# Kernel tuning notes

Hardware: AMD Instinct MI355X
Metric: run time of the kernel (lower is better)

Reference implementation:

```python
import jax, jax.numpy as jnp
import numpy as np

N = 50000      # n_nodes
E = 800000     # n_edges (before self-loops)
IN = 256       # in_channels
MID = 512      # mid_channel
MID2 = MID // 2
OUT = 64       # out_channels


def setup_inputs() -> dict:
    key = jax.random.key(0)
    ks = jax.random.split(key, 16)
    def w(k, shape):
        fan_in = shape[0]
        return jax.random.normal(k, shape, jnp.float32) * (1.0 / np.sqrt(fan_in))
    return {
        "node_feature": jax.random.normal(ks[0], (N, IN), jnp.float32),
        "edge_index": jax.random.randint(ks[1], (2, E), 0, N, jnp.int32),
        # GCNConv weights (PyG convention: x @ W, bias added after aggregation)
        "Wg1": w(ks[2], (IN, MID)),   "bg1": jnp.zeros((MID,), jnp.float32),
        "Wg2": w(ks[3], (MID, MID2)), "bg2": jnp.zeros((MID2,), jnp.float32),
        "Wg3": w(ks[4], (MID2, OUT)), "bg3": jnp.zeros((OUT,), jnp.float32),
        # parallel Linear layers
        "Wl1": w(ks[5], (IN, MID)),   "bl1": jnp.zeros((MID,), jnp.float32),
        "Wl2": w(ks[6], (MID, MID2)), "bl2": jnp.zeros((MID2,), jnp.float32),
        "Wl3": w(ks[7], (MID2, OUT)), "bl3": jnp.zeros((OUT,), jnp.float32),
    }


def reference(node_feature, edge_index, Wg1, bg1, Wg2, bg2, Wg3, bg3,
              Wl1, bl1, Wl2, bl2, Wl3, bl3):
    n = node_feature.shape[0]
    # list_add_self_loops: append (i, i) for every node
    loops = jnp.arange(n, dtype=edge_index.dtype)
    src = jnp.concatenate([edge_index[0], loops])
    dst = jnp.concatenate([edge_index[1], loops])
    # symmetric GCN normalization: deg computed on graph with self-loops
    deg = jax.ops.segment_sum(jnp.ones_like(dst, jnp.float32), dst, num_segments=n)
    dis = jax.lax.rsqrt(jnp.maximum(deg, 1.0))  # deg >= 1 thanks to self-loops
    norm = dis[src] * dis[dst]                  # [E'] edge coefficients

    def gcn_conv(x, W, b):
        h = x @ W                                            # [N, F_out]
        msgs = h[src] * norm[:, None]                        # gather + scale
        return jax.ops.segment_sum(msgs, dst, num_segments=n) + b  # scatter-add

    h1 = jax.nn.elu(gcn_conv(node_feature, Wg1, bg1)) + node_feature @ Wl1 + bl1
    h2 = jax.nn.elu(gcn_conv(h1, Wg2, bg2)) + h1 @ Wl2 + bl2
    out = gcn_conv(h2, Wg3, bg3) + h2 @ Wl3 + bl3
    return out
```

## Files before the change

kernel.cpp:

```cpp
#include <hip/hip_runtime.h>
#include <hip/hip_bf16.h>
#include <math.h>

#define IN_CH  256
#define MID    512
#define MID2   256
#define OUT_CH 64

typedef __attribute__((ext_vector_type(8))) short s16x8;
typedef __attribute__((ext_vector_type(4))) float f32x4;


__global__ __launch_bounds__(256) void deg_kernel(const int* __restrict__ dst,
                                                  int* __restrict__ cnt, int E) {
  int stride = gridDim.x * blockDim.x;
  for (int e = blockIdx.x * blockDim.x + threadIdx.x; e < E; e += stride)
    atomicAdd(&cnt[dst[e]], 1);
}

__global__ __launch_bounds__(1024) void scan_dis_kernel(const int* __restrict__ cnt,
                                                        int* __restrict__ rowstart,
                                                        float* __restrict__ dis, int N) {
  __shared__ int part[1024];
  int t = threadIdx.x;
  int chunk = (N + 1023) >> 10;
  int lo = t * chunk;
  int hi = lo + chunk; if (hi > N) hi = N; if (lo > N) lo = N;
  int s = 0;
  for (int i = lo; i < hi; ++i) s += cnt[i] + 1;
  part[t] = s;
  __syncthreads();
  for (int off = 1; off < 1024; off <<= 1) {
    int v = (t >= off) ? part[t - off] : 0;
    __syncthreads();
    part[t] += v;
    __syncthreads();
  }
  int base = part[t] - s;
  for (int i = lo; i < hi; ++i) {
    int d = cnt[i] + 1;
    rowstart[i] = base;
    dis[i] = rsqrtf((float)d);
    base += d;
  }
  if (t == 1023) rowstart[N] = part[1023];
}

__global__ __launch_bounds__(256) void fill_adj_kernel(const int* __restrict__ src,
                                                       const int* __restrict__ dst,
                                                       const int* __restrict__ rowstart,
                                                       int* __restrict__ cnt2,
                                                       int* __restrict__ adj,
                                                       int E, int N) {
  int total = E + N;
  int stride = gridDim.x * blockDim.x;
  for (int e = blockIdx.x * blockDim.x + threadIdx.x; e < total; e += stride) {
    int s, d;
    if (e < E) { s = src[e]; d = dst[e]; }
    else       { s = d = e - E; }
    int pos = rowstart[d] + atomicAdd(&cnt2[d], 1);
    adj[pos] = s;
  }
}


__device__ inline unsigned bf16_rne(float v) {
  unsigned u = __float_as_uint(v);
  return (u + 0x7FFFu + ((u >> 16) & 1u)) >> 16;
}

__global__ __launch_bounds__(256) void wsplit_cat(const float* __restrict__ W,
                                                  short* __restrict__ Th,
                                                  short* __restrict__ Tl,
                                                  int K, int F, int noff) {
  int idx = blockIdx.x * 256 + threadIdx.x;
  if (idx >= K * F) return;
  int k = idx / F, n = idx - k * F;
  float v = W[idx];
  unsigned h = bf16_rne(v);
  float hf = __uint_as_float(h << 16);
  unsigned l = bf16_rne(v - hf);
  Th[(size_t)(noff + n) * K + k] = (short)h;
  Tl[(size_t)(noff + n) * K + k] = (short)l;
}


template<bool OUT2_BF16>
__global__ __launch_bounds__(256, 2)
void gemm_dual(const float* __restrict__ A, const short* __restrict__ Bth,
               const short* __restrict__ Btl, const float* __restrict__ bias1,
               float* __restrict__ C1, void* __restrict__ C2,
               int Nrows, int K, int F1) {
  __shared__ short lds[4 * 128 * 64];
  short* Ah = lds;
  short* Al = lds + 8192;
  short* Bh = lds + 16384;
  short* Bl = lds + 24576;

  const int tid  = threadIdx.x;
  const int lane = tid & 63;
  const int wid  = tid >> 6;
  const int wr = wid >> 1, wc = wid & 1;
  const int row0 = blockIdx.x * 128;
  const int col0 = blockIdx.y * 128;

  f32x4 acc[4][4] = {};

  const int sr    = tid >> 1;
  const int shalf = (tid & 1) << 5;
  int arow = row0 + sr; if (arow > Nrows - 1) arow = Nrows - 1;
  const float* Abase  = A   + (size_t)arow * K + shalf;
  const short* Bhbase = Bth + (size_t)(col0 + sr) * K + shalf;
  const short* Blbase = Btl + (size_t)(col0 + sr) * K + shalf;
  int wslot[4];
  #pragma unroll
  for (int i = 0; i < 4; ++i)
    wslot[i] = sr * 64 + ((((shalf >> 3) + i) ^ (sr & 7)) << 3);

  for (int k0 = 0; k0 < K; k0 += 64) {
    float4 av[8];
    const float* ap = Abase + k0;
    #pragma unroll
    for (int i = 0; i < 8; ++i) av[i] = *(const float4*)(ap + i * 4);
    s16x8 rbh[4], rbl[4];
    const short* bp = Bhbase + k0;
    const short* bq = Blbase + k0;
    #pragma unroll
    for (int i = 0; i < 4; ++i) rbh[i] = *(const s16x8*)(bp + i * 8);
    #pragma unroll
    for (int i = 0; i < 4; ++i) rbl[i] = *(const s16x8*)(bq + i * 8);

    __syncthreads();

    #pragma unroll
    for (int i = 0; i < 4; ++i) {
      s16x8 hi, lo;
      #pragma unroll
      for (int j = 0; j < 2; ++j) {
        float4 v = av[i * 2 + j];
        float vv[4] = {v.x, v.y, v.z, v.w};
        #pragma unroll
        for (int m = 0; m < 4; ++m) {
          unsigned h = bf16_rne(vv[m]);
          float hf = __uint_as_float(h << 16);
          unsigned l = bf16_rne(vv[m] - hf);
          hi[j * 4 + m] = (short)h;
          lo[j * 4 + m] = (short)l;
        }
      }
      *(s16x8*)(Ah + wslot[i]) = hi;
      *(s16x8*)(Al + wslot[i]) = lo;
    }
    #pragma unroll
    for (int i = 0; i < 4; ++i) {
      *(s16x8*)(Bh + wslot[i]) = rbh[i];
      *(s16x8*)(Bl + wslot[i]) = rbl[i];
    }
    __syncthreads();

    #pragma unroll
    for (int ks = 0; ks < 2; ++ks) {
      const int sw = ((((ks << 2) + (lane >> 4)) ^ (lane & 7)) << 3);
      s16x8 fah[4], fal[4], fbh[4], fbl[4];
      #pragma unroll
      for (int mi = 0; mi < 4; ++mi) {
        int base = (wr * 64 + mi * 16 + (lane & 15)) * 64 + sw;
        fah[mi] = *(const s16x8*)(Ah + base);
        fal[mi] = *(const s16x8*)(Al + base);
      }
      #pragma unroll
      for (int ni = 0; ni < 4; ++ni) {
        int base = (wc * 64 + ni * 16 + (lane & 15)) * 64 + sw;
        fbh[ni] = *(const s16x8*)(Bh + base);
        fbl[ni] = *(const s16x8*)(Bl + base);
      }
      #pragma unroll
      for (int mi = 0; mi < 4; ++mi)
        #pragma unroll
        for (int ni = 0; ni < 4; ++ni) {
          acc[mi][ni] = __builtin_amdgcn_mfma_f32_16x16x32_bf16(fah[mi], fbh[ni], acc[mi][ni], 0, 0, 0);
          acc[mi][ni] = __builtin_amdgcn_mfma_f32_16x16x32_bf16(fah[mi], fbl[ni], acc[mi][ni], 0, 0, 0);
          acc[mi][ni] = __builtin_amdgcn_mfma_f32_16x16x32_bf16(fal[mi], fbh[ni], acc[mi][ni], 0, 0, 0);
        }
    }
  }

  #pragma unroll
  for (int mi = 0; mi < 4; ++mi) {
    #pragma unroll
    for (int r = 0; r < 4; ++r) {
      int rr = row0 + wr * 64 + mi * 16 + (lane >> 4) * 4 + r;
      if (rr >= Nrows) continue;
      #pragma unroll
      for (int ni = 0; ni < 4; ++ni) {
        int cc = col0 + wc * 64 + ni * 16 + (lane & 15);
        float v = acc[mi][ni][r];
        if (cc < F1) {
          C1[(size_t)rr * F1 + cc] = v + bias1[cc];
        } else {
          int c2 = cc - F1;
          if (OUT2_BF16)
            ((unsigned short*)C2)[(size_t)rr * F1 + c2] = (unsigned short)bf16_rne(v);
          else
            ((float*)C2)[(size_t)rr * F1 + c2] = v;
        }
      }
    }
  }
}


template<int F, bool DO_ELU>
__global__ __launch_bounds__(256) void agg_bf16(const unsigned short* __restrict__ H,
                                                const int* __restrict__ adj,
                                                const int* __restrict__ rowstart,
                                                const float* __restrict__ dis,
                                                const float* __restrict__ bias,
                                                float* __restrict__ out, int N) {
  constexpr int VF = F / 64;
  typedef __attribute__((ext_vector_type(VF))) unsigned short uvec;
  int node = (int)((blockIdx.x * blockDim.x + threadIdx.x) >> 6);
  int lane = threadIdx.x & 63;
  if (node >= N) return;
  int e = rowstart[node];
  const int end = rowstart[node + 1];

  float acc[VF] = {};
  const unsigned short* base = H + (size_t)lane * VF;
  for (; e + 4 <= end; e += 4) {
    int s0 = adj[e], s1 = adj[e + 1], s2 = adj[e + 2], s3 = adj[e + 3];
    float w0 = dis[s0], w1 = dis[s1], w2 = dis[s2], w3 = dis[s3];
    uvec v0 = *(const uvec*)(base + (size_t)s0 * F);
    uvec v1 = *(const uvec*)(base + (size_t)s1 * F);
    uvec v2 = *(const uvec*)(base + (size_t)s2 * F);
    uvec v3 = *(const uvec*)(base + (size_t)s3 * F);
    #pragma unroll
    for (int j = 0; j < VF; ++j) {
      acc[j] = fmaf(__uint_as_float((unsigned)v0[j] << 16), w0, acc[j]);
      acc[j] = fmaf(__uint_as_float((unsigned)v1[j] << 16), w1, acc[j]);
      acc[j] = fmaf(__uint_as_float((unsigned)v2[j] << 16), w2, acc[j]);
      acc[j] = fmaf(__uint_as_float((unsigned)v3[j] << 16), w3, acc[j]);
    }
  }
  for (; e < end; ++e) {
    int s = adj[e]; float w = dis[s];
    uvec v = *(const uvec*)(base + (size_t)s * F);
    #pragma unroll
    for (int j = 0; j < VF; ++j)
      acc[j] = fmaf(__uint_as_float((unsigned)v[j] << 16), w, acc[j]);
  }

  float di = dis[node];
  float* op = out + (size_t)node * F + lane * VF;
  const float* bp = bias + lane * VF;
  #pragma unroll
  for (int j = 0; j < VF; ++j) {
    float val = fmaf(acc[j], di, bp[j]);
    if (DO_ELU) val = (val > 0.f) ? val : expm1f(val);
    op[j] += val;
  }
}


template<int F, bool DO_ELU>
__global__ __launch_bounds__(256) void agg_f32(const float* __restrict__ H,
                                               const int* __restrict__ adj,
                                               const int* __restrict__ rowstart,
                                               const float* __restrict__ dis,
                                               const float* __restrict__ bias,
                                               float* __restrict__ out, int N) {
  int node = (int)((blockIdx.x * blockDim.x + threadIdx.x) >> 6);
  int lane = threadIdx.x & 63;
  if (node >= N) return;
  int e = rowstart[node];
  const int end = rowstart[node + 1];
  float acc = 0.f;
  for (; e + 4 <= end; e += 4) {
    int s0 = adj[e], s1 = adj[e + 1], s2 = adj[e + 2], s3 = adj[e + 3];
    float w0 = dis[s0], w1 = dis[s1], w2 = dis[s2], w3 = dis[s3];
    float q0 = H[(size_t)s0 * F + lane], q1 = H[(size_t)s1 * F + lane];
    float q2 = H[(size_t)s2 * F + lane], q3 = H[(size_t)s3 * F + lane];
    acc = fmaf(q0, w0, acc); acc = fmaf(q1, w1, acc);
    acc = fmaf(q2, w2, acc); acc = fmaf(q3, w3, acc);
  }
  for (; e < end; ++e) {
    int s = adj[e];
    acc = fmaf(H[(size_t)s * F + lane], dis[s], acc);
  }
  float val = fmaf(acc, dis[node], bias[lane]);
  if (DO_ELU) val = (val > 0.f) ? val : expm1f(val);
  out[(size_t)node * F + lane] += val;
}


static inline char* ws_align(char*& ws, size_t bytes) {
  ws = (char*)(((uintptr_t)ws + 63) & ~(uintptr_t)63);
  char* p = ws;
  ws += bytes;
  return p;
}

extern "C" void kernel_launch(void* const* d_in, const int* in_sizes, int n_in,
                              void* d_out, int out_size, void* d_ws, size_t ws_size,
                              hipStream_t stream) {
  const float* x   = (const float*)d_in[0];
  const int*  eidx = (const int*)d_in[1];
  const float* Wg1 = (const float*)d_in[2];
  const float* bg1 = (const float*)d_in[3];
  const float* Wg2 = (const float*)d_in[4];
  const float* bg2 = (const float*)d_in[5];
  const float* Wg3 = (const float*)d_in[6];
  const float* bg3 = (const float*)d_in[7];
  const float* Wl1 = (const float*)d_in[8];
  const float* bl1 = (const float*)d_in[9];
  const float* Wl2 = (const float*)d_in[10];
  const float* bl2 = (const float*)d_in[11];
  const float* Wl3 = (const float*)d_in[12];
  const float* bl3 = (const float*)d_in[13];

  const int N = in_sizes[0] / IN_CH;
  const int E = in_sizes[1] / 2;
  const int* esrc = eidx;
  const int* edst = eidx + E;

  char* ws = (char*)d_ws;
  float* h1   = (float*)ws_align(ws, (size_t)N * MID  * 4);
  float* h2   = (float*)ws_align(ws, (size_t)N * MID2 * 4);
  unsigned short* Hbf = (unsigned short*)ws_align(ws, (size_t)N * MID * 2);
  float* Hb3  = (float*)ws_align(ws, (size_t)N * OUT_CH * 4);
  float* dis      = (float*)ws_align(ws, (size_t)N * 4);
  int*   rowstart = (int*)ws_align(ws, (size_t)(N + 1) * 4);
  int*   cnt      = (int*)ws_align(ws, (size_t)N * 4);
  int*   cnt2     = (int*)ws_align(ws, (size_t)N * 4);
  int*   adj      = (int*)ws_align(ws, (size_t)(E + N) * 4);
  short* w1h = (short*)ws_align(ws, (size_t)1024 * IN_CH * 2);
  short* w1l = (short*)ws_align(ws, (size_t)1024 * IN_CH * 2);
  short* w2h = (short*)ws_align(ws, (size_t)512 * MID * 2);
  short* w2l = (short*)ws_align(ws, (size_t)512 * MID * 2);
  short* w3h = (short*)ws_align(ws, (size_t)128 * MID2 * 2);
  short* w3l = (short*)ws_align(ws, (size_t)128 * MID2 * 2);

  hipMemsetAsync(cnt, 0, (size_t)N * 4, stream);
  hipMemsetAsync(cnt2, 0, (size_t)N * 4, stream);
  deg_kernel<<<1024, 256, 0, stream>>>(edst, cnt, E);
  scan_dis_kernel<<<1, 1024, 0, stream>>>(cnt, rowstart, dis, N);
  fill_adj_kernel<<<2048, 256, 0, stream>>>(esrc, edst, rowstart, cnt2, adj, E, N);

  {
    int n1 = IN_CH * MID, n2 = MID * MID2, n3 = MID2 * OUT_CH;
    wsplit_cat<<<(n1 + 255) / 256, 256, 0, stream>>>(Wl1, w1h, w1l, IN_CH, MID, 0);
    wsplit_cat<<<(n1 + 255) / 256, 256, 0, stream>>>(Wg1, w1h, w1l, IN_CH, MID, MID);
    wsplit_cat<<<(n2 + 255) / 256, 256, 0, stream>>>(Wl2, w2h, w2l, MID, MID2, 0);
    wsplit_cat<<<(n2 + 255) / 256, 256, 0, stream>>>(Wg2, w2h, w2l, MID, MID2, MID2);
    wsplit_cat<<<(n3 + 255) / 256, 256, 0, stream>>>(Wl3, w3h, w3l, MID2, OUT_CH, 0);
    wsplit_cat<<<(n3 + 255) / 256, 256, 0, stream>>>(Wg3, w3h, w3l, MID2, OUT_CH, OUT_CH);
  }

  const int aggBlocks = (N + 3) / 4;
  const int rowBlocks = (N + 127) / 128;

  dim3 g1(rowBlocks, (2 * MID) / 128);
  gemm_dual<true><<<g1, 256, 0, stream>>>(x, w1h, w1l, bl1, h1, Hbf, N, IN_CH, MID);
  agg_bf16<MID, true><<<aggBlocks, 256, 0, stream>>>(Hbf, adj, rowstart, dis, bg1, h1, N);

  dim3 g2(rowBlocks, (2 * MID2) / 128);
  gemm_dual<true><<<g2, 256, 0, stream>>>(h1, w2h, w2l, bl2, h2, Hbf, N, MID, MID2);
  agg_bf16<MID2, true><<<aggBlocks, 256, 0, stream>>>(Hbf, adj, rowstart, dis, bg2, h2, N);

  float* outp = (float*)d_out;
  dim3 g3(rowBlocks, (2 * OUT_CH) / 128);
  gemm_dual<false><<<g3, 256, 0, stream>>>(h2, w3h, w3l, bl3, outp, Hb3, N, MID2, OUT_CH);
  agg_f32<OUT_CH, false><<<aggBlocks, 256, 0, stream>>>(Hb3, adj, rowstart, dis, bg3, outp, N);
}
```

Baseline: 894.0 us.

## Aggregate layer-1 input before GEMM and pre-split activations into bf16 pairs

Layer 1 now aggregates the 256-wide input features over the graph first, then multiplies by Wg1 (A·X·W instead of A·(X·W)). This halves the gather width of the first aggregation, from 512 to 256 channels. The linear and GCN branches of layer 1 become two separate GEMMs, and the second one fuses ELU, the residual add and the hi/lo bf16 split in its epilogue. Activations are stored pre-split as hi/lo bf16 pairs, so the GEMMs no longer convert fp32 to bf16 in their inner loop. The trade-off is more intermediate buffers and traffic, workspace aliasing that must stay correct, and a different rounding path because the aggregated input is quantised to a bf16 pair.

After: 871.2 us. 2.6% less time.

```diff
diff --git a/kernel.cpp b/kernel.cpp
--- a/kernel.cpp
+++ b/kernel.cpp
@@ -8,6 +8,8 @@
 #define OUT_CH 64
 
 typedef __attribute__((ext_vector_type(8))) short s16x8;
+typedef __attribute__((ext_vector_type(8))) unsigned short u16x8;
+typedef __attribute__((ext_vector_type(4))) unsigned short u16x4;
 typedef __attribute__((ext_vector_type(4))) float f32x4;
 
 
@@ -70,8 +72,8 @@
 }
 
 __global__ __launch_bounds__(256) void wsplit_cat(const float* __restrict__ W,
-                                                  short* __restrict__ Th,
-                                                  short* __restrict__ Tl,
+                                                  unsigned short* __restrict__ Th,
+                                                  unsigned short* __restrict__ Tl,
                                                   int K, int F, int noff) {
   int idx = blockIdx.x * 256 + threadIdx.x;
   if (idx >= K * F) return;
@@ -80,22 +82,47 @@
   unsigned h = bf16_rne(v);
   float hf = __uint_as_float(h << 16);
   unsigned l = bf16_rne(v - hf);
-  Th[(size_t)(noff + n) * K + k] = (short)h;
-  Tl[(size_t)(noff + n) * K + k] = (short)l;
-}
-
-
-template<bool OUT2_BF16>
+  Th[(size_t)(noff + n) * K + k] = (unsigned short)h;
+  Tl[(size_t)(noff + n) * K + k] = (unsigned short)l;
+}
+
+__global__ __launch_bounds__(256) void split_pair(const float* __restrict__ X,
+                                                  unsigned short* __restrict__ Xh,
+                                                  unsigned short* __restrict__ Xl,
+                                                  int n8) {
+  int i = blockIdx.x * 256 + threadIdx.x;
+  if (i >= n8) return;
+  const float4* xp = (const float4*)X + (size_t)i * 2;
+  float4 a = xp[0], b = xp[1];
+  float vv[8] = {a.x, a.y, a.z, a.w, b.x, b.y, b.z, b.w};
+  u16x8 hv, lv;
+  #pragma unroll
+  for (int j = 0; j < 8; ++j) {
+    unsigned h = bf16_rne(vv[j]);
+    float hf = __uint_as_float(h << 16);
+    unsigned l = bf16_rne(vv[j] - hf);
+    hv[j] = (unsigned short)h;
+    lv[j] = (unsigned short)l;
+  }
+  ((u16x8*)Xh)[i] = hv;
+  ((u16x8*)Xl)[i] = lv;
+}
+
+
+template<int MODE>
 __global__ __launch_bounds__(256, 2)
-void gemm_dual(const float* __restrict__ A, const short* __restrict__ Bth,
-               const short* __restrict__ Btl, const float* __restrict__ bias1,
-               float* __restrict__ C1, void* __restrict__ C2,
-               int Nrows, int K, int F1) {
-  __shared__ short lds[4 * 128 * 64];
-  short* Ah = lds;
-  short* Al = lds + 8192;
-  short* Bh = lds + 16384;
-  short* Bl = lds + 24576;
+void gemm_ps(const unsigned short* __restrict__ Agh, const unsigned short* __restrict__ Agl,
+             const unsigned short* __restrict__ Bgh, const unsigned short* __restrict__ Bgl,
+             const float* __restrict__ bias,
+             const float* __restrict__ C1r, float* __restrict__ C1w,
+             unsigned short* __restrict__ O2h, unsigned short* __restrict__ O2l,
+             float* __restrict__ O2f,
+             int Nrows, int K, int F1) {
+  __shared__ unsigned short lds[4 * 128 * 64];
+  unsigned short* Ah = lds;
+  unsigned short* Al = lds + 8192;
+  unsigned short* Bh = lds + 16384;
+  unsigned short* Bl = lds + 24576;
 
   const int tid  = threadIdx.x;
   const int lane = tid & 63;
@@ -109,52 +136,33 @@
   const int sr    = tid >> 1;
   const int shalf = (tid & 1) << 5;
   int arow = row0 + sr; if (arow > Nrows - 1) arow = Nrows - 1;
-  const float* Abase  = A   + (size_t)arow * K + shalf;
-  const short* Bhbase = Bth + (size_t)(col0 + sr) * K + shalf;
-  const short* Blbase = Btl + (size_t)(col0 + sr) * K + shalf;
+  const unsigned short* Ahb = Agh + (size_t)arow * K + shalf;
+  const unsigned short* Alb = Agl + (size_t)arow * K + shalf;
+  const unsigned short* Bhb = Bgh + (size_t)(col0 + sr) * K + shalf;
+  const unsigned short* Blb = Bgl + (size_t)(col0 + sr) * K + shalf;
   int wslot[4];
   #pragma unroll
   for (int i = 0; i < 4; ++i)
     wslot[i] = sr * 64 + ((((shalf >> 3) + i) ^ (sr & 7)) << 3);
 
   for (int k0 = 0; k0 < K; k0 += 64) {
-    float4 av[8];
-    const float* ap = Abase + k0;
-    #pragma unroll
-    for (int i = 0; i < 8; ++i) av[i] = *(const float4*)(ap + i * 4);
-    s16x8 rbh[4], rbl[4];
-    const short* bp = Bhbase + k0;
-    const short* bq = Blbase + k0;
-    #pragma unroll
-    for (int i = 0; i < 4; ++i) rbh[i] = *(const s16x8*)(bp + i * 8);
-    #pragma unroll
-    for (int i = 0; i < 4; ++i) rbl[i] = *(const s16x8*)(bq + i * 8);
+    u16x8 rah[4], ral[4], rbh[4], rbl[4];
+    #pragma unroll
+    for (int i = 0; i < 4; ++i) rah[i] = *(const u16x8*)(Ahb + k0 + i * 8);
+    #pragma unroll
+    for (int i = 0; i < 4; ++i) ral[i] = *(const u16x8*)(Alb + k0 + i * 8);
+    #pragma unroll
+    for (int i = 0; i < 4; ++i) rbh[i] = *(const u16x8*)(Bhb + k0 + i * 8);
+    #pragma unroll
+    for (int i = 0; i < 4; ++i) rbl[i] = *(const u16x8*)(Blb + k0 + i * 8);
 
     __syncthreads();
-
     #pragma unroll
     for (int i = 0; i < 4; ++i) {
-      s16x8 hi, lo;
-      #pragma unroll
-      for (int j = 0; j < 2; ++j) {
-        float4 v = av[i * 2 + j];
-        float vv[4] = {v.x, v.y, v.z, v.w};
-        #pragma unroll
-        for (int m = 0; m < 4; ++m) {
-          unsigned h = bf16_rne(vv[m]);
-          float hf = __uint_as_float(h << 16);
-          unsigned l = bf16_rne(vv[m] - hf);
-          hi[j * 4 + m] = (short)h;
-          lo[j * 4 + m] = (short)l;
-        }
-      }
-      *(s16x8*)(Ah + wslot[i]) = hi;
-      *(s16x8*)(Al + wslot[i]) = lo;
-    }
-    #pragma unroll
-    for (int i = 0; i < 4; ++i) {
-      *(s16x8*)(Bh + wslot[i]) = rbh[i];
-      *(s16x8*)(Bl + wslot[i]) = rbl[i];
+      *(u16x8*)(Ah + wslot[i]) = rah[i];
+      *(u16x8*)(Al + wslot[i]) = ral[i];
+      *(u16x8*)(Bh + wslot[i]) = rbh[i];
+      *(u16x8*)(Bl + wslot[i]) = rbl[i];
     }
     __syncthreads();
 
@@ -195,14 +203,26 @@
       for (int ni = 0; ni < 4; ++ni) {
         int cc = col0 + wc * 64 + ni * 16 + (lane & 15);
         float v = acc[mi][ni][r];
-        if (cc < F1) {
-          C1[(size_t)rr * F1 + cc] = v + bias1[cc];
+        if (MODE == 0) {
+          C1w[(size_t)rr * F1 + cc] = v + bias[cc];
+        } else if (MODE == 1) {
+          float t = v + bias[cc];
+          t = (t > 0.f) ? t : expm1f(t);
+          t += C1r[(size_t)rr * F1 + cc];
+          size_t idx = (size_t)rr * F1 + cc;
+          unsigned h = bf16_rne(t);
+          float hf = __uint_as_float(h << 16);
+          unsigned l = bf16_rne(t - hf);
+          O2h[idx] = (unsigned short)h;
+          O2l[idx] = (unsigned short)l;
         } else {
-          int c2 = cc - F1;
-          if (OUT2_BF16)
-            ((unsigned short*)C2)[(size_t)rr * F1 + c2] = (unsigned short)bf16_rne(v);
-          else
-            ((float*)C2)[(size_t)rr * F1 + c2] = v;
+          if (cc < F1) {
+            C1w[(size_t)rr * F1 + cc] = v + bias[cc];
+          } else {
+            size_t idx = (size_t)rr * F1 + (cc - F1);
+            if (MODE == 2) O2h[idx] = (unsigned short)bf16_rne(v);
+            else           O2f[idx] = v;
+          }
         }
       }
     }
@@ -210,13 +230,13 @@
 }
 
 
-template<int F, bool DO_ELU>
-__global__ __launch_bounds__(256) void agg_bf16(const unsigned short* __restrict__ H,
-                                                const int* __restrict__ adj,
-                                                const int* __restrict__ rowstart,
-                                                const float* __restrict__ dis,
-                                                const float* __restrict__ bias,
-                                                float* __restrict__ out, int N) {
+template<int F>
+__global__ __launch_bounds__(256) void agg_split(const unsigned short* __restrict__ H,
+                                                 const int* __restrict__ adj,
+                                                 const int* __restrict__ rowstart,
+                                                 const float* __restrict__ dis,
+                                                 unsigned short* __restrict__ Zh,
+                                                 unsigned short* __restrict__ Zl, int N) {
   constexpr int VF = F / 64;
   typedef __attribute__((ext_vector_type(VF))) unsigned short uvec;
   int node = (int)((blockIdx.x * blockDim.x + threadIdx.x) >> 6);
@@ -251,18 +271,82 @@
   }
 
   float di = dis[node];
-  float* op = out + (size_t)node * F + lane * VF;
+  uvec hv, lv;
+  #pragma unroll
+  for (int j = 0; j < VF; ++j) {
+    float val = acc[j] * di;
+    unsigned h = bf16_rne(val);
+    float hf = __uint_as_float(h << 16);
+    unsigned l = bf16_rne(val - hf);
+    hv[j] = (unsigned short)h;
+    lv[j] = (unsigned short)l;
+  }
+  *(uvec*)(Zh + (size_t)node * F + lane * VF) = hv;
+  *(uvec*)(Zl + (size_t)node * F + lane * VF) = lv;
+}
+
+template<int F>
+__global__ __launch_bounds__(256) void agg_addsplit(const unsigned short* __restrict__ H,
+                                                    const int* __restrict__ adj,
+                                                    const int* __restrict__ rowstart,
+                                                    const float* __restrict__ dis,
+                                                    const float* __restrict__ bias,
+                                                    const float* __restrict__ lin,
+                                                    unsigned short* __restrict__ Zh,
+                                                    unsigned short* __restrict__ Zl, int N) {
+  constexpr int VF = F / 64;
+  typedef __attribute__((ext_vector_type(VF))) unsigned short uvec;
+  int node = (int)((blockIdx.x * blockDim.x + threadIdx.x) >> 6);
+  int lane = threadIdx.x & 63;
+  if (node >= N) return;
+  int e = rowstart[node];
+  const int end = rowstart[node + 1];
+
+  float acc[VF] = {};
+  const unsigned short* base = H + (size_t)lane * VF;
+  for (; e + 4 <= end; e += 4) {
+    int s0 = adj[e], s1 = adj[e + 1], s2 = adj[e + 2], s3 = adj[e + 3];
+    float w0 = dis[s0], w1 = dis[s1], w2 = dis[s2], w3 = dis[s3];
+    uvec v0 = *(const uvec*)(base + (size_t)s0 * F);
+    uvec v1 = *(const uvec*)(base + (size_t)s1 * F);
+    uvec v2 = *(const uvec*)(base + (size_t)s2 * F);
+    uvec v3 = *(const uvec*)(base + (size_t)s3 * F);
+    #pragma unroll
+    for (int j = 0; j < VF; ++j) {
+      acc[j] = fmaf(__uint_as_float((unsigned)v0[j] << 16), w0, acc[j]);
+      acc[j] = fmaf(__uint_as_float((unsigned)v1[j] << 16), w1, acc[j]);
+      acc[j] = fmaf(__uint_as_float((unsigned)v2[j] << 16), w2, acc[j]);
+      acc[j] = fmaf(__uint_as_float((unsigned)v3[j] << 16), w3, acc[j]);
+    }
+  }
+  for (; e < end; ++e) {
+    int s = adj[e]; float w = dis[s];
+    uvec v = *(const uvec*)(base + (size_t)s * F);
+    #pragma unroll
+    for (int j = 0; j < VF; ++j)
+      acc[j] = fmaf(__uint_as_float((unsigned)v[j] << 16), w, acc[j]);
+  }
+
+  float di = dis[node];
   const float* bp = bias + lane * VF;
+  const float* lp = lin + (size_t)node * F + lane * VF;
+  uvec hv, lv;
   #pragma unroll
   for (int j = 0; j < VF; ++j) {
     float val = fmaf(acc[j], di, bp[j]);
-    if (DO_ELU) val = (val > 0.f) ? val : expm1f(val);
-    op[j] += val;
-  }
-}
-
-
-template<int F, bool DO_ELU>
+    val = (val > 0.f) ? val : expm1f(val);
+    val += lp[j];
+    unsigned h = bf16_rne(val);
+    float hf = __uint_as_float(h << 16);
+    unsigned l = bf16_rne(val - hf);
+    hv[j] = (unsigned short)h;
+    lv[j] = (unsigned short)l;
+  }
+  *(uvec*)(Zh + (size_t)node * F + lane * VF) = hv;
+  *(uvec*)(Zl + (size_t)node * F + lane * VF) = lv;
+}
+
+template<int F>
 __global__ __launch_bounds__(256) void agg_f32(const float* __restrict__ H,
                                                const int* __restrict__ adj,
                                                const int* __restrict__ rowstart,
@@ -287,14 +371,12 @@
     int s = adj[e];
     acc = fmaf(H[(size_t)s * F + lane], dis[s], acc);
   }
-  float val = fmaf(acc, dis[node], bias[lane]);
-  if (DO_ELU) val = (val > 0.f) ? val : expm1f(val);
-  out[(size_t)node * F + lane] += val;
+  out[(size_t)node * F + lane] += fmaf(acc, dis[node], bias[lane]);
 }
 
 
 static inline char* ws_align(char*& ws, size_t bytes) {
-  ws = (char*)(((uintptr_t)ws + 63) & ~(uintptr_t)63);
+  ws = (char*)(((uintptr_t)ws + 255) & ~(uintptr_t)255);
   char* p = ws;
   ws += bytes;
   return p;
@@ -324,21 +406,29 @@
   const int* edst = eidx + E;
 
   char* ws = (char*)d_ws;
-  float* h1   = (float*)ws_align(ws, (size_t)N * MID  * 4);
-  float* h2   = (float*)ws_align(ws, (size_t)N * MID2 * 4);
-  unsigned short* Hbf = (unsigned short*)ws_align(ws, (size_t)N * MID * 2);
-  float* Hb3  = (float*)ws_align(ws, (size_t)N * OUT_CH * 4);
+  unsigned short* xh = (unsigned short*)ws_align(ws, (size_t)N * IN_CH * 2);
+  unsigned short* xl = (unsigned short*)ws_align(ws, (size_t)N * IN_CH * 2);
+  unsigned short* h1h = xh;
+  unsigned short* zh = (unsigned short*)ws_align(ws, (size_t)N * IN_CH * 2);
+  unsigned short* zl = (unsigned short*)ws_align(ws, (size_t)N * IN_CH * 2);
+  float* h2lin = (float*)zh;
+  float* h1lin = (float*)ws_align(ws, (size_t)N * MID * 4);
+  unsigned short* Hbf = (unsigned short*)h1lin;
+  unsigned short* h2h = (unsigned short*)((char*)h1lin + (size_t)N * MID2 * 2);
+  unsigned short* h2l = (unsigned short*)((char*)h1lin + (size_t)N * MID2 * 4);
+  float*          Hb3 = (float*)((char*)h1lin + (size_t)N * MID2 * 6);
+  unsigned short* h1l = (unsigned short*)ws_align(ws, (size_t)N * MID * 2);
   float* dis      = (float*)ws_align(ws, (size_t)N * 4);
   int*   rowstart = (int*)ws_align(ws, (size_t)(N + 1) * 4);
   int*   cnt      = (int*)ws_align(ws, (size_t)N * 4);
   int*   cnt2     = (int*)ws_align(ws, (size_t)N * 4);
   int*   adj      = (int*)ws_align(ws, (size_t)(E + N) * 4);
-  short* w1h = (short*)ws_align(ws, (size_t)1024 * IN_CH * 2);
-  short* w1l = (short*)ws_align(ws, (size_t)1024 * IN_CH * 2);
-  short* w2h = (short*)ws_align(ws, (size_t)512 * MID * 2);
-  short* w2l = (short*)ws_align(ws, (size_t)512 * MID * 2);
-  short* w3h = (short*)ws_align(ws, (size_t)128 * MID2 * 2);
-  short* w3l = (short*)ws_align(ws, (size_t)128 * MID2 * 2);
+  unsigned short* w1h = (unsigned short*)ws_align(ws, (size_t)1024 * IN_CH * 2);
+  unsigned short* w1l = (unsigned short*)ws_align(ws, (size_t)1024 * IN_CH * 2);
+  unsigned short* w2h = (unsigned short*)ws_align(ws, (size_t)512 * MID * 2);
+  unsigned short* w2l = (unsigned short*)ws_align(ws, (size_t)512 * MID * 2);
+  unsigned short* w3h = (unsigned short*)ws_align(ws, (size_t)128 * MID2 * 2);
+  unsigned short* w3l = (unsigned short*)ws_align(ws, (size_t)128 * MID2 * 2);
 
   hipMemsetAsync(cnt, 0, (size_t)N * 4, stream);
   hipMemsetAsync(cnt2, 0, (size_t)N * 4, stream);
@@ -356,19 +446,33 @@
     wsplit_cat<<<(n3 + 255) / 256, 256, 0, stream>>>(Wg3, w3h, w3l, MID2, OUT_CH, OUT_CH);
   }
 
+  {
+    int n8 = N * IN_CH / 8;
+    split_pair<<<(n8 + 255) / 256, 256, 0, stream>>>(x, xh, xl, n8);
+  }
+
   const int aggBlocks = (N + 3) / 4;
   const int rowBlocks = (N + 127) / 128;
-
-  dim3 g1(rowBlocks, (2 * MID) / 128);
-  gemm_dual<true><<<g1, 256, 0, stream>>>(x, w1h, w1l, bl1, h1, Hbf, N, IN_CH, MID);
-  agg_bf16<MID, true><<<aggBlocks, 256, 0, stream>>>(Hbf, adj, rowstart, dis, bg1, h1, N);
+  float* outp = (float*)d_out;
+
+  agg_split<IN_CH><<<aggBlocks, 256, 0, stream>>>(xh, adj, rowstart, dis, zh, zl, N);
+  dim3 g1(rowBlocks, MID / 128);
+  gemm_ps<0><<<g1, 256, 0, stream>>>(xh, xl, w1h, w1l, bl1,
+                                     nullptr, h1lin, nullptr, nullptr, nullptr,
+                                     N, IN_CH, MID);
+  gemm_ps<1><<<g1, 256, 0, stream>>>(zh, zl, w1h + (size_t)MID * IN_CH, w1l + (size_t)MID * IN_CH, bg1,
+                                     h1lin, nullptr, h1h, h1l, nullptr,
+                                     N, IN_CH, MID);
 
   dim3 g2(rowBlocks, (2 * MID2) / 128);
-  gemm_dual<true><<<g2, 256, 0, stream>>>(h1, w2h, w2l, bl2, h2, Hbf, N, MID, MID2);
-  agg_bf16<MID2, true><<<aggBlocks, 256, 0, stream>>>(Hbf, adj, rowstart, dis, bg2, h2, N);
-
-  float* outp = (float*)d_out;
+  gemm_ps<2><<<g2, 256, 0, stream>>>(h1h, h1l, w2h, w2l, bl2,
+                                     nullptr, h2lin, Hbf, nullptr, nullptr,
+                                     N, MID, MID2);
+  agg_addsplit<MID2><<<aggBlocks, 256, 0, stream>>>(Hbf, adj, rowstart, dis, bg2, h2lin, h2h, h2l, N);
+
   dim3 g3(rowBlocks, (2 * OUT_CH) / 128);
-  gemm_dual<false><<<g3, 256, 0, stream>>>(h2, w3h, w3l, bl3, outp, Hb3, N, MID2, OUT_CH);
-  agg_f32<OUT_CH, false><<<aggBlocks, 256, 0, stream>>>(Hb3, adj, rowstart, dis, bg3, outp, N);
-}
+  gemm_ps<3><<<g3, 256, 0, stream>>>(h2h, h2l, w3h, w3l, bl3,
+                                     nullptr, outp, nullptr, nullptr, Hb3,
+                                     N, MID2, OUT_CH);
+  agg_f32<OUT_CH><<<aggBlocks, 256, 0, stream>>>(Hb3, adj, rowstart, dis, bg3, outp, N);
+}
```
